# Kernel optimization log

Measured on AMD Instinct MI355X. Metric: run time of the kernel, lower is better.

Reference implementation:

```python
import jax, jax.numpy as jnp
import numpy as np


def setup_inputs() -> dict:
    key = jax.random.key(0)
    T, B, E, H = 512, 64, 512, 1024
    ks = jax.random.split(key, 14)
    bound = 1.0 / np.sqrt(H)
    u = lambda k, shape: jax.random.uniform(k, shape, jnp.float32, -bound, bound)
    return {
        "embeds": jax.random.normal(ks[0], (T, B, E), jnp.float32),
        "W_fx": u(ks[1], (E, H)), "W_fh": u(ks[2], (H, H)), "b_f": u(ks[3], (H,)) + 1.0,
        "W_ix": u(ks[4], (E, H)), "W_ih": u(ks[5], (H, H)), "b_i": u(ks[6], (H,)),
        "W_gx": u(ks[7], (E, H)), "W_gh": u(ks[8], (H, H)), "b_g": u(ks[9], (H,)),
        "W_ox": u(ks[10], (E, H)), "W_oh": u(ks[11], (H, H)), "b_o": u(ks[12], (H,)),
    }


def reference(embeds, W_fx, W_fh, b_f, W_ix, W_ih, b_i, W_gx, W_gh, b_g, W_ox, W_oh, b_o):
    T, B, E = embeds.shape
    H = W_fh.shape[0]
    # Precompute input projections for all gates in one fused GEMM: [T,B,4H]
    Wx = jnp.concatenate([W_gx, W_ix, W_fx, W_ox], axis=1)  # [E,4H]
    Wh = jnp.concatenate([W_gh, W_ih, W_fh, W_oh], axis=1)  # [H,4H]
    b = jnp.concatenate([b_g, b_i, b_f, b_o])               # [4H]
    x_proj = jnp.einsum('tbe,ef->tbf', embeds, Wx) + b      # [T,B,4H]

    def step(carry, xp):
        h_t, c_t = carry
        z = xp + h_t @ Wh                                   # [B,4H]
        g = jnp.tanh(z[:, 0 * H:1 * H])
        i = jax.nn.sigmoid(z[:, 1 * H:2 * H])
        f = jax.nn.sigmoid(z[:, 2 * H:3 * H])
        o = jax.nn.sigmoid(z[:, 3 * H:4 * H])
        c_t = g * i + c_t * f
        h_t = jnp.tanh(c_t) * o
        return (h_t, c_t), h_t

    h0 = jnp.zeros((B, H), embeds.dtype)
    c0 = jnp.zeros((B, H), embeds.dtype)
    (h_last, _), h_arr = jax.lax.scan(step, (h0, c0), x_proj)
    return (h_arr, h_last)
```

## Files before the change

### kernel.cpp

```cpp
#include <hip/hip_runtime.h>

typedef _Float16 f16;
typedef _Float16 f16x8 __attribute__((ext_vector_type(8)));
typedef float f32x4 __attribute__((ext_vector_type(4)));

#define AS1 __attribute__((address_space(1)))
#define AS3 __attribute__((address_space(3)))

__device__ __forceinline__ void gload_lds16(const void* g, void* l) {
  __builtin_amdgcn_global_load_lds((const AS1 void*)g, (AS3 void*)l, 16, 0, 0);
}

__global__ __launch_bounds__(256) void conv_f32_f16(const float* __restrict__ in,
                                                    f16* __restrict__ out, int n8) {
  int i = blockIdx.x * 256 + threadIdx.x;
  if (i >= n8) return;
  const float4* in4 = (const float4*)in;
  float4 a = in4[i * 2], b = in4[i * 2 + 1];
  f16x8 o = {(f16)a.x, (f16)a.y, (f16)a.z, (f16)a.w,
             (f16)b.x, (f16)b.y, (f16)b.z, (f16)b.w};
  *(f16x8*)(out + (size_t)i * 8) = o;
}

__global__ __launch_bounds__(256) void transp_wx(const float* __restrict__ src,
                                                 f16* __restrict__ dst, int gbase) {
  __shared__ float tile[32][33];
  const int tx = threadIdx.x, ty = threadIdx.y;
  const int c0 = blockIdx.x * 32, r0 = blockIdx.y * 32;
#pragma unroll
  for (int i = 0; i < 4; ++i)
    tile[ty + i * 8][tx] = src[(size_t)(r0 + ty + i * 8) * 1024 + c0 + tx];
  __syncthreads();
#pragma unroll
  for (int i = 0; i < 4; ++i) {
    int c = c0 + ty + i * 8;
    dst[(size_t)(gbase + c) * 512 + r0 + tx] = (f16)tile[tx][ty + i * 8];
  }
}

__global__ __launch_bounds__(256) void transp_wh(const float* __restrict__ src,
                                                 f16* __restrict__ dst, int g) {
  __shared__ float tile[32][33];
  const int tx = threadIdx.x, ty = threadIdx.y;
  const int c0 = blockIdx.x * 32, r0 = blockIdx.y * 32;
#pragma unroll
  for (int i = 0; i < 4; ++i)
    tile[ty + i * 8][tx] = src[(size_t)(r0 + ty + i * 8) * 1024 + c0 + tx];
  __syncthreads();
#pragma unroll
  for (int i = 0; i < 4; ++i) {
    int uu = c0 + ty + i * 8;
    int drow = (uu >> 4) * 64 + g * 16 + (uu & 15);
    dst[(size_t)drow * 1024 + r0 + tx] = (f16)tile[tx][ty + i * 8];
  }
}

__global__ __launch_bounds__(256) void pack_bias(const float* __restrict__ bg,
                                                 const float* __restrict__ bi,
                                                 const float* __restrict__ bf,
                                                 const float* __restrict__ bo,
                                                 float* __restrict__ bc) {
  int n = blockIdx.x * 256 + threadIdx.x;
  int i = n & 1023;
  float v;
  if (n < 1024) v = bg[i];
  else if (n < 2048) v = bi[i];
  else if (n < 3072) v = bf[i];
  else v = bo[i];
  bc[n] = v;
}

__global__ __launch_bounds__(256) void gemm_xproj(const f16* __restrict__ A,
                                                  const f16* __restrict__ Bt,
                                                  const float* __restrict__ bias,
                                                  f16* __restrict__ C) {
  __shared__ f16 As[128 * 64];
  __shared__ f16 Bs[128 * 64];
  const int tid = threadIdx.x;
  const int l = tid & 63, wv = tid >> 6, lq = l >> 4, lr = l & 15;
  const int m0 = blockIdx.x * 128, n0 = blockIdx.y * 128;
  const int wrow = (wv >> 1) * 64, wcol = (wv & 1) * 64;
  f32x4 acc[4][4] = {};
  const int rA = tid >> 3, cA = (tid & 7) * 8;
  for (int kk = 0; kk < 8; ++kk) {
#pragma unroll
    for (int i = 0; i < 4; ++i) {
      gload_lds16(A + (size_t)(m0 + rA + i * 32) * 512 + kk * 64 + cA,
                  (char*)As + wv * 1024 + i * 4096);
      gload_lds16(Bt + (size_t)(n0 + rA + i * 32) * 512 + kk * 64 + cA,
                  (char*)Bs + wv * 1024 + i * 4096);
    }
    __syncthreads();
#pragma unroll
    for (int ks = 0; ks < 2; ++ks) {
      f16x8 a[4], b[4];
#pragma unroll
      for (int mt = 0; mt < 4; ++mt)
        a[mt] = *(const f16x8*)(As + (wrow + mt * 16 + lr) * 64 + ks * 32 + lq * 8);
#pragma unroll
      for (int nt = 0; nt < 4; ++nt)
        b[nt] = *(const f16x8*)(Bs + (wcol + nt * 16 + lr) * 64 + ks * 32 + lq * 8);
#pragma unroll
      for (int mt = 0; mt < 4; ++mt)
#pragma unroll
        for (int nt = 0; nt < 4; ++nt)
          acc[mt][nt] = __builtin_amdgcn_mfma_f32_16x16x32_f16(a[mt], b[nt], acc[mt][nt], 0, 0, 0);
    }
    __syncthreads();
  }
  float bb[4];
#pragma unroll
  for (int nt = 0; nt < 4; ++nt) bb[nt] = bias[n0 + wcol + nt * 16 + lr];
#pragma unroll
  for (int mt = 0; mt < 4; ++mt)
#pragma unroll
    for (int nt = 0; nt < 4; ++nt)
#pragma unroll
      for (int j = 0; j < 4; ++j) {
        int row = m0 + wrow + mt * 16 + lq * 4 + j;
        int col = n0 + wcol + nt * 16 + lr;
        C[(size_t)row * 4096 + col] = (f16)(acc[mt][nt][j] + bb[nt]);
      }
}

__global__ __launch_bounds__(1024) void lstm_rec(const f16* __restrict__ whP,
                                                 const f16* __restrict__ xp,
                                                 f16* __restrict__ hbuf,
                                                 float* __restrict__ out,
                                                 unsigned int* __restrict__ flags) {
  extern __shared__ char smem[];
  const int tid = threadIdx.x, wg = blockIdx.x;
  const int l = tid & 63, wv = tid >> 6, lq = l >> 4, lr = l & 15;
  const int rg = wv & 3, ks = wv >> 2;
  const int b = tid >> 4, u = tid & 15;
  {
    const char* src = (const char*)(whP + (size_t)wg * 65536);
#pragma unroll
    for (int i = 0; i < 8; ++i) {
      int lin = (tid + i * 1024) * 16;
      int c = lin >> 11;
      uint4 v = *(const uint4*)(src + lin);
      *(uint4*)(smem + (lin ^ ((c & 7) << 4))) = v;
    }
  }
  float* Z = (float*)(smem + 131072);
  float c_state = 0.f;
  const int arow = rg * 16 + lr;
  const int kbase = ks * 512 + lq * 16;
  float xg[4];
  {
    const f16* xrow = xp + (size_t)b * 4096 + wg * 16 + u;
#pragma unroll
    for (int g = 0; g < 4; ++g) xg[g] = (float)xrow[g * 1024];
  }
  __syncthreads();
  for (int t = 0; t < 512; ++t) {
    const char* hsrc = (const char*)hbuf + (t & 1) * 131072 + arow * 2048 + kbase;
    unsigned long long pre[16];
#pragma unroll
    for (int kk = 0; kk < 8; ++kk) {
      pre[kk * 2] = __hip_atomic_load((const unsigned long long*)(hsrc + kk * 64),
                                      __ATOMIC_RELAXED, __HIP_MEMORY_SCOPE_AGENT);
      pre[kk * 2 + 1] = __hip_atomic_load((const unsigned long long*)(hsrc + kk * 64 + 8),
                                          __ATOMIC_RELAXED, __HIP_MEMORY_SCOPE_AGENT);
    }
    f32x4 acc[4] = {{0.f, 0.f, 0.f, 0.f}, {0.f, 0.f, 0.f, 0.f},
                    {0.f, 0.f, 0.f, 0.f}, {0.f, 0.f, 0.f, 0.f}};
#pragma unroll
    for (int kk = 0; kk < 8; ++kk) {
      union { unsigned long long q[2]; f16x8 v; } au;
      au.q[0] = pre[kk * 2]; au.q[1] = pre[kk * 2 + 1];
#pragma unroll
      for (int cc = 0; cc < 4; ++cc) {
        int col = cc * 16 + lr;
        f16x8 bv = *(const f16x8*)(smem + ((col * 2048 + kbase + kk * 64) ^ ((col & 7) << 4)));
        acc[cc] = __builtin_amdgcn_mfma_f32_16x16x32_f16(au.v, bv, acc[cc], 0, 0, 0);
      }
    }
#define ZP(cc, j) (Z + (rg * 16 + lq * 4 + (j)) * 66 + (cc) * 16 + lr)
    if (ks == 3) {
#pragma unroll
      for (int cc = 0; cc < 4; ++cc)
#pragma unroll
        for (int j = 0; j < 4; ++j) *ZP(cc, j) = acc[cc][j];
    }
    __syncthreads();
    if (ks == 2) {
#pragma unroll
      for (int cc = 0; cc < 4; ++cc)
#pragma unroll
        for (int j = 0; j < 4; ++j) *ZP(cc, j) += acc[cc][j];
    }
    __syncthreads();
    if (ks == 1) {
#pragma unroll
      for (int cc = 0; cc < 4; ++cc)
#pragma unroll
        for (int j = 0; j < 4; ++j) *ZP(cc, j) += acc[cc][j];
    }
    __syncthreads();
    if (ks == 0) {
#pragma unroll
      for (int cc = 0; cc < 4; ++cc)
#pragma unroll
        for (int j = 0; j < 4; ++j) *ZP(cc, j) += acc[cc][j];
    }
    __syncthreads();
#undef ZP
    float z0 = Z[b * 66 + u] + xg[0];
    float z1 = Z[b * 66 + 16 + u] + xg[1];
    float z2 = Z[b * 66 + 32 + u] + xg[2];
    float z3 = Z[b * 66 + 48 + u] + xg[3];
    float gv = tanhf(z0);
    float iv = 1.f / (1.f + __expf(-z1));
    float fv = 1.f / (1.f + __expf(-z2));
    float ov = 1.f / (1.f + __expf(-z3));
    c_state = gv * iv + c_state * fv;
    float hv = tanhf(c_state) * ov;
    unsigned short hu = __builtin_bit_cast(unsigned short, (f16)hv);
    unsigned other = (unsigned)__shfl_xor((int)(unsigned)hu, 1, 64);
    f16* hdst = hbuf + ((t + 1) & 1) * 65536;
    if (!(u & 1))
      __hip_atomic_store((unsigned*)(hdst + b * 1024 + wg * 16 + u),
                         ((unsigned)hu) | (other << 16),
                         __ATOMIC_RELAXED, __HIP_MEMORY_SCOPE_AGENT);
    asm volatile("s_waitcnt vmcnt(0)" ::: "memory");
    __syncthreads();
    if (tid == 0)
      __hip_atomic_store(&flags[wg], (unsigned)(t + 1), __ATOMIC_RELAXED, __HIP_MEMORY_SCOPE_AGENT);
    const int hcol = wg * 16 + u;
    out[((size_t)t * 64 + b) * 1024 + hcol] = hv;
    if (t == 511) {
      out[(size_t)33554432 + b * 1024 + hcol] = hv;
    } else {
      const f16* xrow = xp + ((size_t)(t + 1) * 64 + b) * 4096 + wg * 16 + u;
#pragma unroll
      for (int g = 0; g < 4; ++g) xg[g] = (float)xrow[g * 1024];
    }
    if (tid < 64)
      while (__hip_atomic_load(&flags[tid], __ATOMIC_RELAXED, __HIP_MEMORY_SCOPE_AGENT) <
             (unsigned)(t + 1))
        __builtin_amdgcn_s_sleep(1);
    __syncthreads();
    asm volatile("" ::: "memory");
  }
}

extern "C" void kernel_launch(void* const* d_in, const int* in_sizes, int n_in,
                              void* d_out, int out_size, void* d_ws, size_t ws_size,
                              hipStream_t stream) {
  const float* embeds = (const float*)d_in[0];
  const float* W_fx = (const float*)d_in[1];
  const float* W_fh = (const float*)d_in[2];
  const float* b_f  = (const float*)d_in[3];
  const float* W_ix = (const float*)d_in[4];
  const float* W_ih = (const float*)d_in[5];
  const float* b_i  = (const float*)d_in[6];
  const float* W_gx = (const float*)d_in[7];
  const float* W_gh = (const float*)d_in[8];
  const float* b_g  = (const float*)d_in[9];
  const float* W_ox = (const float*)d_in[10];
  const float* W_oh = (const float*)d_in[11];
  const float* b_o  = (const float*)d_in[12];

  char* ws = (char*)d_ws;
  f16*   xproj = (f16*)(ws + 0);
  f16*   embF  = (f16*)(ws + 268435456);
  f16*   wxT   = (f16*)(ws + 301989888);
  f16*   whP   = (f16*)(ws + 306184192);
  float* bcat  = (float*)(ws + 314572800);
  f16*   hbuf  = (f16*)(ws + 314589184);
  unsigned int* flags = (unsigned int*)(ws + 314851328);
  if (ws_size < 314851584ull) return;

  hipMemsetAsync(hbuf, 0, 262144 + 256, stream);

  conv_f32_f16<<<8192, 256, 0, stream>>>(embeds, embF, 2097152);
  const float* wxs[4] = {W_gx, W_ix, W_fx, W_ox};
  const float* whs[4] = {W_gh, W_ih, W_fh, W_oh};
  for (int g = 0; g < 4; ++g) {
    transp_wx<<<dim3(32, 16), dim3(32, 8), 0, stream>>>(wxs[g], wxT, g * 1024);
    transp_wh<<<dim3(32, 32), dim3(32, 8), 0, stream>>>(whs[g], whP, g);
  }
  pack_bias<<<16, 256, 0, stream>>>(b_g, b_i, b_f, b_o, bcat);
  gemm_xproj<<<dim3(256, 32), 256, 0, stream>>>(embF, wxT, bcat, xproj);

  hipFuncSetAttribute((const void*)lstm_rec, hipFuncAttributeMaxDynamicSharedMemorySize, 147968);
  lstm_rec<<<64, 1024, 147968, stream>>>(whP, xproj, hbuf, (float*)d_out, flags);
}
```

Baseline: 5.830 ms.

## Replace flag barrier with sentinel-tagged h buffers and atomic LDS reduction

Removes the per-step global flag barrier across the 64 workgroups. Consumers now poll the h values themselves, which are tagged with a 0xFEFEFEFE sentinel in a 4-deep ring buffer, and each slot is reset two steps ahead. The serial three-stage LDS reduction is replaced with LDS atomicAdd, and the xproj output is re-laid out so each workgroup's four gate values sit contiguously. The aim is to cut cross-workgroup synchronisation latency on every recurrent step. The risk is that an f16 pair could legitimately equal the sentinel bit pattern, and the polling relies on ordering of relaxed atomics.

```diff
diff --git a/kernel.cpp b/kernel.cpp
--- a/kernel.cpp
+++ b/kernel.cpp
@@ -119,15 +119,15 @@
       for (int j = 0; j < 4; ++j) {
         int row = m0 + wrow + mt * 16 + lq * 4 + j;
         int col = n0 + wcol + nt * 16 + lr;
-        C[(size_t)row * 4096 + col] = (f16)(acc[mt][nt][j] + bb[nt]);
+        int g = col >> 10, wg2 = (col >> 4) & 63, u2 = col & 15;
+        C[(size_t)row * 4096 + wg2 * 64 + g * 16 + u2] = (f16)(acc[mt][nt][j] + bb[nt]);
       }
 }
 
 __global__ __launch_bounds__(1024) void lstm_rec(const f16* __restrict__ whP,
-                                                 const f16* __restrict__ xp,
+                                                 const f16* __restrict__ xq,
                                                  f16* __restrict__ hbuf,
-                                                 float* __restrict__ out,
-                                                 unsigned int* __restrict__ flags) {
+                                                 float* __restrict__ out) {
   extern __shared__ char smem[];
   const int tid = threadIdx.x, wg = blockIdx.x;
   const int l = tid & 63, wv = tid >> 6, lq = l >> 4, lr = l & 15;
@@ -149,20 +149,38 @@
   const int kbase = ks * 512 + lq * 16;
   float xg[4];
   {
-    const f16* xrow = xp + (size_t)b * 4096 + wg * 16 + u;
-#pragma unroll
-    for (int g = 0; g < 4; ++g) xg[g] = (float)xrow[g * 1024];
+    const f16* xrow = xq + (size_t)b * 4096 + wg * 64 + u;
+#pragma unroll
+    for (int g = 0; g < 4; ++g) xg[g] = (float)xrow[g * 16];
   }
   __syncthreads();
   for (int t = 0; t < 512; ++t) {
-    const char* hsrc = (const char*)hbuf + (t & 1) * 131072 + arow * 2048 + kbase;
+    {
+      f16* rbuf = hbuf + ((t + 2) & 3) * 65536;
+      if (!(u & 1))
+        __hip_atomic_store((unsigned*)(rbuf + b * 1024 + wg * 16 + u), 0xFEFEFEFEu,
+                           __ATOMIC_RELAXED, __HIP_MEMORY_SCOPE_AGENT);
+    }
+    const char* hsrc = (const char*)hbuf + (t & 3) * 131072 + arow * 2048 + kbase;
     unsigned long long pre[16];
-#pragma unroll
-    for (int kk = 0; kk < 8; ++kk) {
-      pre[kk * 2] = __hip_atomic_load((const unsigned long long*)(hsrc + kk * 64),
-                                      __ATOMIC_RELAXED, __HIP_MEMORY_SCOPE_AGENT);
-      pre[kk * 2 + 1] = __hip_atomic_load((const unsigned long long*)(hsrc + kk * 64 + 8),
-                                          __ATOMIC_RELAXED, __HIP_MEMORY_SCOPE_AGENT);
+    while (true) {
+#pragma unroll
+      for (int kk = 0; kk < 8; ++kk) {
+        pre[kk * 2] = __hip_atomic_load((const unsigned long long*)(hsrc + kk * 64),
+                                        __ATOMIC_RELAXED, __HIP_MEMORY_SCOPE_AGENT);
+        pre[kk * 2 + 1] = __hip_atomic_load((const unsigned long long*)(hsrc + kk * 64 + 8),
+                                            __ATOMIC_RELAXED, __HIP_MEMORY_SCOPE_AGENT);
+      }
+      asm volatile("s_waitcnt vmcnt(0)" ::: "memory");
+      int ok = 1;
+#pragma unroll
+      for (int kk = 0; kk < 16; ++kk) {
+        unsigned lo = (unsigned)pre[kk], hi = (unsigned)(pre[kk] >> 32);
+        ok &= (lo != 0xFEFEFEFEu);
+        ok &= (hi != 0xFEFEFEFEu);
+      }
+      if (__all(ok)) break;
+      __builtin_amdgcn_s_sleep(1);
     }
     f32x4 acc[4] = {{0.f, 0.f, 0.f, 0.f}, {0.f, 0.f, 0.f, 0.f},
                     {0.f, 0.f, 0.f, 0.f}, {0.f, 0.f, 0.f, 0.f}};
@@ -185,25 +203,11 @@
         for (int j = 0; j < 4; ++j) *ZP(cc, j) = acc[cc][j];
     }
     __syncthreads();
-    if (ks == 2) {
+    if (ks != 3) {
 #pragma unroll
       for (int cc = 0; cc < 4; ++cc)
 #pragma unroll
-        for (int j = 0; j < 4; ++j) *ZP(cc, j) += acc[cc][j];
-    }
-    __syncthreads();
-    if (ks == 1) {
-#pragma unroll
-      for (int cc = 0; cc < 4; ++cc)
-#pragma unroll
-        for (int j = 0; j < 4; ++j) *ZP(cc, j) += acc[cc][j];
-    }
-    __syncthreads();
-    if (ks == 0) {
-#pragma unroll
-      for (int cc = 0; cc < 4; ++cc)
-#pragma unroll
-        for (int j = 0; j < 4; ++j) *ZP(cc, j) += acc[cc][j];
+        for (int j = 0; j < 4; ++j) atomicAdd(ZP(cc, j), acc[cc][j]);
     }
     __syncthreads();
 #undef ZP
@@ -211,6 +215,7 @@
     float z1 = Z[b * 66 + 16 + u] + xg[1];
     float z2 = Z[b * 66 + 32 + u] + xg[2];
     float z3 = Z[b * 66 + 48 + u] + xg[3];
+    __syncthreads();
     float gv = tanhf(z0);
     float iv = 1.f / (1.f + __expf(-z1));
     float fv = 1.f / (1.f + __expf(-z2));
@@ -219,30 +224,20 @@
     float hv = tanhf(c_state) * ov;
     unsigned short hu = __builtin_bit_cast(unsigned short, (f16)hv);
     unsigned other = (unsigned)__shfl_xor((int)(unsigned)hu, 1, 64);
-    f16* hdst = hbuf + ((t + 1) & 1) * 65536;
+    f16* hdst = hbuf + ((t + 1) & 3) * 65536;
     if (!(u & 1))
       __hip_atomic_store((unsigned*)(hdst + b * 1024 + wg * 16 + u),
                          ((unsigned)hu) | (other << 16),
                          __ATOMIC_RELAXED, __HIP_MEMORY_SCOPE_AGENT);
-    asm volatile("s_waitcnt vmcnt(0)" ::: "memory");
-    __syncthreads();
-    if (tid == 0)
-      __hip_atomic_store(&flags[wg], (unsigned)(t + 1), __ATOMIC_RELAXED, __HIP_MEMORY_SCOPE_AGENT);
     const int hcol = wg * 16 + u;
     out[((size_t)t * 64 + b) * 1024 + hcol] = hv;
     if (t == 511) {
       out[(size_t)33554432 + b * 1024 + hcol] = hv;
     } else {
-      const f16* xrow = xp + ((size_t)(t + 1) * 64 + b) * 4096 + wg * 16 + u;
-#pragma unroll
-      for (int g = 0; g < 4; ++g) xg[g] = (float)xrow[g * 1024];
-    }
-    if (tid < 64)
-      while (__hip_atomic_load(&flags[tid], __ATOMIC_RELAXED, __HIP_MEMORY_SCOPE_AGENT) <
-             (unsigned)(t + 1))
-        __builtin_amdgcn_s_sleep(1);
-    __syncthreads();
-    asm volatile("" ::: "memory");
+      const f16* xrow = xq + ((size_t)(t + 1) * 64 + b) * 4096 + wg * 64 + u;
+#pragma unroll
+      for (int g = 0; g < 4; ++g) xg[g] = (float)xrow[g * 16];
+    }
   }
 }
 
@@ -269,11 +264,8 @@
   f16*   wxT   = (f16*)(ws + 301989888);
   f16*   whP   = (f16*)(ws + 306184192);
   float* bcat  = (float*)(ws + 314572800);
-  f16*   hbuf  = (f16*)(ws + 314589184);
-  unsigned int* flags = (unsigned int*)(ws + 314851328);
-  if (ws_size < 314851584ull) return;
-
-  hipMemsetAsync(hbuf, 0, 262144 + 256, stream);
+  f16*   hbuf  = (f16*)(ws + 268435456);
+  if (ws_size < 314589184ull) return;
 
   conv_f32_f16<<<8192, 256, 0, stream>>>(embeds, embF, 2097152);
   const float* wxs[4] = {W_gx, W_ix, W_fx, W_ox};
@@ -285,6 +277,9 @@
   pack_bias<<<16, 256, 0, stream>>>(b_g, b_i, b_f, b_o, bcat);
   gemm_xproj<<<dim3(256, 32), 256, 0, stream>>>(embF, wxT, bcat, xproj);
 
+  hipMemsetAsync(hbuf, 0, 131072, stream);
+  hipMemsetAsync((char*)hbuf + 131072, 0xFE, 393216, stream);
+
   hipFuncSetAttribute((const void*)lstm_rec, hipFuncAttributeMaxDynamicSharedMemorySize, 147968);
-  lstm_rec<<<64, 1024, 147968, stream>>>(whP, xproj, hbuf, (float*)d_out, flags);
-}
+  lstm_rec<<<64, 1024, 147968, stream>>>(whP, xproj, hbuf, (float*)d_out);
+}
```

Result: slower. 14.46 ms (+148.0%).
